# Performance work log

Hardware: AMD Instinct MI355X
Metric: run time of the kernel (lower is better)

The kernel has to match this reference:

```python
import jax, jax.numpy as jnp
import numpy as np

N = 1600        # brain parcellation nodes
MAXD = 500      # delay-buffer length
B = 4           # batches
DT = 0.05
T_STEPS = 500   # steps per batch

# theta layout (ModelParams means):
# 0 std_in, 1 W_E, 2 tau_E, 3 gamma_E, 4 W_I, 5 tau_I, 6 I_0, 7 g,
# 8 g_EE, 9 g_IE, 10 g_EI, 11 aE, 12 bE, 13 dE, 14 aI, 15 bI, 16 dI
THETA = np.array([0.02, 1.0, 100.0, 0.641/1000.0, 0.7, 10.0, 0.32, 20.0,
                  0.1, 0.1, 0.1, 310.0, 125.0, 0.16, 615.0, 177.0, 0.087],
                 dtype=np.float32)


def h_tf(a, b, d, current):
    u = a * current - b
    num = 1e-5 + jnp.abs(u)
    den = 1e-5 * d + jnp.abs(1.0 - jnp.exp(-d * u))
    return num / (den + 1e-8)


def setup_inputs() -> dict:
    key = jax.random.key(0)
    k0, k1, k2, k3, k4 = jax.random.split(key, 5)
    SC = jax.random.uniform(k0, (N, N), dtype=jnp.float32) / N  # normalized connectivity
    L = jnp.diag(SC.sum(axis=1)) - SC                           # graph Laplacian D - SC
    x0 = 0.1 * jax.random.uniform(k1, (N, 2), dtype=jnp.float32)
    hE = 0.1 * jax.random.uniform(k2, (N, MAXD), dtype=jnp.float32)
    delays = jax.random.randint(k3, (N, N), 0, MAXD)
    noise_raw = jax.random.normal(k4, (B, N, 2), dtype=jnp.float32)
    theta = jnp.asarray(THETA)
    return {"x0": x0, "hE": hE, "L": L, "theta": theta,
            "noise_raw": noise_raw, "delays": delays, "batches": B}


def reference(x0, hE, L, theta, noise_raw, delays, batches):
    (std_in, W_E, tau_E, gamma_E, W_I, tau_I, I_0, g,
     g_EE, g_IE, g_EI, aE, bE, dE_c, aI, bI, dI_c) = [theta[i] for i in range(17)]

    def run_batch(x, hEb, noise):
        def step(carry, _):
            x, hEc = carry
            E = x[:, 0:1]
            I = x[:, 1:2]
            # delay gather: out[i,j] = hE[i, delays[i,j]], then mean over j
            delayed_E = jnp.take_along_axis(hEc, delays, axis=1).mean(axis=1, keepdims=True)
            I_E = W_E * I_0 + g_EE * E + g * (L @ delayed_E) - g_IE * I
            I_I = W_I * I_0 + g_EI * E - I
            R_E = h_tf(aE, bE, dE_c, I_E)
            R_I = h_tf(aI, bI, dI_c, I_I)
            dE = -E / tau_E + (1.0 - E) * gamma_E * R_E
            dI = -I / tau_I + R_I
            x_new = x + DT * jnp.concatenate([dE, dI], axis=1) + noise
            hE_new = jnp.concatenate([x_new[:, 0:1], hEc[:, :-1]], axis=1)
            return (x_new, hE_new), x_new

        (x_f, hE_f), ys = jax.lax.scan(step, (x, hEb), None, length=T_STEPS - 1)
        X = jnp.concatenate([x[None], ys], axis=0)  # (T, N, 2)
        return X, x_f, hE_f

    sdt = std_in * jnp.sqrt(jnp.float32(DT))
    x = x0
    Xs = []
    for b in range(batches):  # small fixed count of sequential batches
        X, x, hE = run_batch(x, hE, noise_raw[b] * sdt)
        Xs.append(X)
    X_all = jnp.concatenate(Xs, axis=0)  # (batches*T, N, 2)
    return X_all, x, hE
```

## Files before the change

kernel.cpp:

```cpp
#include <hip/hip_runtime.h>
#include <math.h>

#define NN 1600
#define MAXD 500
#define TS 500
#define NBATCH 4
#define GBLK 100
#define WAVES 4
#define NWAVE (GBLK * WAVES)
#define RPW 4
#define NFLAG 512
#define DT 0.05f

typedef unsigned int u32;


#define ATSF(p,v)  __hip_atomic_store((p), (v), __ATOMIC_RELAXED, __HIP_MEMORY_SCOPE_AGENT)
#define ATSU(p,v)  __hip_atomic_store((p), (v), __ATOMIC_RELAXED, __HIP_MEMORY_SCOPE_AGENT)

__device__ __forceinline__ float h_tf_dev(float a, float b, float d, float c) {
    float u   = a * c - b;
    float num = 1e-5f + fabsf(u);
    float den = 1e-5f * d + fabsf(1.0f - expf(-d * u));
    return num / (den + 1e-8f);
}

__global__ void cnt_kernel(const int* __restrict__ delays, float* __restrict__ cnt) {
    __shared__ int hist[MAXD];
    const int i = blockIdx.x;
    for (int d = threadIdx.x; d < MAXD; d += blockDim.x) hist[d] = 0;
    __syncthreads();
    const int* row = delays + (size_t)i * NN;
    for (int j = threadIdx.x; j < NN; j += blockDim.x) atomicAdd(&hist[row[j]], 1);
    __syncthreads();
    for (int d = threadIdx.x; d < MAXD; d += blockDim.x)
        cnt[(size_t)i * MAXD + d] = (float)hist[d];
}

__global__ void init_kernel(const float* __restrict__ hE, const float* __restrict__ cnt,
                            float* __restrict__ Hc, float* deT, u32* flags) {
    const int i = blockIdx.x;
    const int lane = threadIdx.x;
    float s = 0.f;
    for (int d = lane; d < MAXD; d += 64) {
        float v = hE[(size_t)i * MAXD + d];
        Hc[(size_t)i * MAXD + d] = v;
        s = fmaf(cnt[(size_t)i * MAXD + d], v, s);
    }
    #pragma unroll
    for (int off = 32; off; off >>= 1) s += __shfl_xor(s, off);
    if (lane == 0) ATSF(&deT[i], s / 1600.0f);
    if (i == 0) {
        for (int k = lane; k < NFLAG; k += 64)
            ATSU(&flags[k], (k < NWAVE) ? 0u : 0x7FFFFFFFu);
    }
}

#define ISSUE_DE() do { \
    asm volatile("global_load_dwordx4 %0, %1, off sc0 sc1" : "=v"(q0) : "v"(src + (lane*4         )) : "memory"); \
    asm volatile("global_load_dwordx4 %0, %1, off sc0 sc1" : "=v"(q1) : "v"(src + (lane*4 + 1*256)) : "memory"); \
    asm volatile("global_load_dwordx4 %0, %1, off sc0 sc1" : "=v"(q2) : "v"(src + (lane*4 + 2*256)) : "memory"); \
    asm volatile("global_load_dwordx4 %0, %1, off sc0 sc1" : "=v"(q3) : "v"(src + (lane*4 + 3*256)) : "memory"); \
    asm volatile("global_load_dwordx4 %0, %1, off sc0 sc1" : "=v"(q4) : "v"(src + (lane*4 + 4*256)) : "memory"); \
    asm volatile("global_load_dwordx4 %0, %1, off sc0 sc1" : "=v"(q5) : "v"(src + (lane*4 + 5*256)) : "memory"); \
    asm volatile("global_load_dword %0, %1, off sc0 sc1"   : "=v"(qx) : "v"(src + (1536 + lane   )) : "memory"); \
} while (0)

__global__ __launch_bounds__(256, 1) void dmf_main(
        const float* __restrict__ x0, const float* __restrict__ L,
        const float* __restrict__ theta, const float* __restrict__ noise,
        float* __restrict__ out, const float* __restrict__ cnt,
        float* __restrict__ Hc, float* deT, u32* flags) {
    const int lane = threadIdx.x & 63;
    const int wv   = __builtin_amdgcn_readfirstlane(threadIdx.x >> 6);
    const int widx = blockIdx.x * WAVES + wv;
    const int base = widx * RPW;

    const float std_in = theta[0],  W_E = theta[1],  tau_E = theta[2], gamma_E = theta[3];
    const float W_I = theta[4],     tau_I = theta[5], I_0 = theta[6],  g = theta[7];
    const float g_EE = theta[8],    g_IE = theta[9], g_EI = theta[10];
    const float aE = theta[11], bE = theta[12], dEc = theta[13];
    const float aI = theta[14], bI = theta[15], dIc = theta[16];
    const float sdt = std_in * sqrtf(DT);

    float E = 0.f, I = 0.f, cnt0 = 0.f;
    float* Hmy = Hc;
    if (lane < RPW) {
        const int i = base + lane;
        E = x0[i * 2 + 0];
        I = x0[i * 2 + 1];
        cnt0 = cnt[(size_t)i * MAXD];
        Hmy = Hc + (size_t)i * MAXD;
    }

    float creg[8][RPW];
    #pragma unroll
    for (int k = 0; k < 8; ++k) {
        const int d = lane + k * 64;
        #pragma unroll
        for (int r = 0; r < RPW; ++r)
            creg[k][r] = (d >= 1 && d < MAXD) ? cnt[(size_t)(base + r) * MAXD + d] : 0.f;
    }

    float4 Lreg[RPW][6];
    float  Ltail[RPW];
    #pragma unroll
    for (int r = 0; r < RPW; ++r) {
        #pragma unroll
        for (int k = 0; k < 6; ++k)
            Lreg[r][k] = *(const float4*)&L[(size_t)(base + r) * NN + lane * 4 + k * 256];
        Ltail[r] = L[(size_t)(base + r) * NN + 1536 + lane];
    }

    const u32* fp1 = flags + lane * 4;
    const u32* fp2 = flags + 256 + lane * 4;

    int h = 0;
    u32 e = 0;

    for (int b = 0; b < NBATCH; ++b) {
        float nE = 0.f, nI = 0.f;
        if (lane < RPW) {
            const int i = base + lane;
            nE = noise[((size_t)b * NN + i) * 2 + 0] * sdt;
            nI = noise[((size_t)b * NN + i) * 2 + 1] * sdt;
            ((float2*)out)[(size_t)b * TS * NN + i] = make_float2(E, I);
        }

        for (int t = 1; t < TS; ++t) {
            h = (h == 0) ? (MAXD - 1) : (h - 1);

            float s[RPW];
            #pragma unroll
            for (int r = 0; r < RPW; ++r) s[r] = 0.f;
            #pragma unroll
            for (int k = 0; k < 8; ++k) {
                const int d = lane + k * 64;
                if (d < MAXD) {
                    int hd = h + d; if (hd >= MAXD) hd -= MAXD;
                    #pragma unroll
                    for (int r = 0; r < RPW; ++r)
                        s[r] = fmaf(creg[k][r], Hc[(size_t)(base + r) * MAXD + hd], s[r]);
                }
            }
            #pragma unroll
            for (int off = 32; off; off >>= 1) {
                #pragma unroll
                for (int r = 0; r < RPW; ++r) s[r] += __shfl_xor(s[r], off);
            }
            float sv = s[0];
            #pragma unroll
            for (int r = 1; r < RPW; ++r) sv = (lane == r) ? s[r] : sv;

            {
                const u32 tgt = e;
                for (;;) {
                    uint4 f1, f2;
                    asm volatile("global_load_dwordx4 %0, %1, off sc0 sc1"
                                 : "=v"(f1) : "v"(fp1) : "memory");
                    asm volatile("global_load_dwordx4 %0, %1, off sc0 sc1"
                                 : "=v"(f2) : "v"(fp2) : "memory");
                    asm volatile("s_waitcnt vmcnt(0)" ::: "memory");
                    __builtin_amdgcn_sched_barrier(0);
                    const bool ok = (f1.x >= tgt) & (f1.y >= tgt) & (f1.z >= tgt) & (f1.w >= tgt)
                                  & (f2.x >= tgt) & (f2.y >= tgt) & (f2.z >= tgt) & (f2.w >= tgt);
                    if (__all(ok)) break;
                    __builtin_amdgcn_s_sleep(1);
                }
            }

            const float* src = deT + (size_t)(e & 1) * NN;
            float4 q0, q1, q2, q3, q4, q5;
            float  qx;
            ISSUE_DE();
            asm volatile("s_waitcnt vmcnt(0)" ::: "memory");
            __builtin_amdgcn_sched_barrier(0);

            float p[RPW];
            #pragma unroll
            for (int r = 0; r < RPW; ++r) {
                float acc = 0.f;
                acc = fmaf(Lreg[r][0].x, q0.x, acc); acc = fmaf(Lreg[r][0].y, q0.y, acc);
                acc = fmaf(Lreg[r][0].z, q0.z, acc); acc = fmaf(Lreg[r][0].w, q0.w, acc);
                acc = fmaf(Lreg[r][1].x, q1.x, acc); acc = fmaf(Lreg[r][1].y, q1.y, acc);
                acc = fmaf(Lreg[r][1].z, q1.z, acc); acc = fmaf(Lreg[r][1].w, q1.w, acc);
                acc = fmaf(Lreg[r][2].x, q2.x, acc); acc = fmaf(Lreg[r][2].y, q2.y, acc);
                acc = fmaf(Lreg[r][2].z, q2.z, acc); acc = fmaf(Lreg[r][2].w, q2.w, acc);
                acc = fmaf(Lreg[r][3].x, q3.x, acc); acc = fmaf(Lreg[r][3].y, q3.y, acc);
                acc = fmaf(Lreg[r][3].z, q3.z, acc); acc = fmaf(Lreg[r][3].w, q3.w, acc);
                acc = fmaf(Lreg[r][4].x, q4.x, acc); acc = fmaf(Lreg[r][4].y, q4.y, acc);
                acc = fmaf(Lreg[r][4].z, q4.z, acc); acc = fmaf(Lreg[r][4].w, q4.w, acc);
                acc = fmaf(Lreg[r][5].x, q5.x, acc); acc = fmaf(Lreg[r][5].y, q5.y, acc);
                acc = fmaf(Lreg[r][5].z, q5.z, acc); acc = fmaf(Lreg[r][5].w, q5.w, acc);
                acc = fmaf(Ltail[r], qx, acc);
                p[r] = acc;
            }
            #pragma unroll
            for (int off = 32; off; off >>= 1) {
                #pragma unroll
                for (int r = 0; r < RPW; ++r) p[r] += __shfl_xor(p[r], off);
            }
            float pv = p[0];
            #pragma unroll
            for (int r = 1; r < RPW; ++r) pv = (lane == r) ? p[r] : pv;

            float2 xi;
            if (lane < RPW) {
                const float IE = W_E * I_0 + g_EE * E + g * pv - g_IE * I;
                const float II = W_I * I_0 + g_EI * E - I;
                const float RE = h_tf_dev(aE, bE, dEc, IE);
                const float RI = h_tf_dev(aI, bI, dIc, II);
                const float dEd = -E / tau_E + (1.0f - E) * gamma_E * RE;
                const float dId = -I / tau_I + RI;
                E = E + DT * dEd + nE;
                I = I + DT * dId + nI;
                ATSF(&deT[(size_t)((e + 1) & 1) * NN + base + lane],
                     (sv + cnt0 * E) * (1.0f / 1600.0f));
                xi = make_float2(E, I);
            }
            asm volatile("s_waitcnt vmcnt(0)" ::: "memory");
            __builtin_amdgcn_sched_barrier(0);
            if (lane == 0) ATSU(&flags[widx], e + 1);
            if (lane < RPW) {
                Hmy[h] = E;
                ((float2*)out)[(size_t)(b * TS + t) * NN + base + lane] = xi;
            }
            ++e;
        }
    }

    const size_t xo2 = (size_t)NBATCH * TS * NN;
    if (lane < RPW)
        ((float2*)out)[xo2 + base + lane] = make_float2(E, I);
    const size_t ho = 2 * xo2 + 2 * NN;
    #pragma unroll
    for (int k = 0; k < 8; ++k) {
        const int d = lane + k * 64;
        if (d < MAXD) {
            int hd = h + d; if (hd >= MAXD) hd -= MAXD;
            #pragma unroll
            for (int r = 0; r < RPW; ++r)
                out[ho + (size_t)(base + r) * MAXD + d] =
                    Hc[(size_t)(base + r) * MAXD + hd];
        }
    }
}

extern "C" void kernel_launch(void* const* d_in, const int* in_sizes, int n_in,
                              void* d_out, int out_size, void* d_ws, size_t ws_size,
                              hipStream_t stream) {
    const float* x0     = (const float*)d_in[0];
    const float* hE     = (const float*)d_in[1];
    const float* L      = (const float*)d_in[2];
    const float* theta  = (const float*)d_in[3];
    const float* noise  = (const float*)d_in[4];
    const int*   delays = (const int*)d_in[5];
    float* out = (float*)d_out;

    float* ws  = (float*)d_ws;
    float* cnt = ws;
    float* Hc  = ws + 800000;
    float* deT = ws + 1600000;
    u32*   flags = (u32*)(ws + 1603200);

    cnt_kernel<<<NN, 256, 0, stream>>>(delays, cnt);
    init_kernel<<<NN, 64, 0, stream>>>(hE, cnt, Hc, deT, flags);
    dmf_main<<<GBLK, 256, 0, stream>>>(x0, L, theta, noise, out, cnt, Hc, deT, flags);
}
```

Before: 5.584 ms.

## Tag delayed-E values with parity bits to overlap data loads with flag polling

Each published deT value now carries a parity tag in its mantissa LSB that encodes the step generation. This lets every wave issue its deT loads at the top of the step, ahead of the local delay sum and the flag wait. The flag loads are also issued early, at the end of the previous step. After the flag barrier the wave checks the tags and re-issues the deT loads only if any value is stale, so the load latency overlaps with other work instead of adding a serial round-trip. The cost is one mantissa bit of precision in the delayed-E means and a possible extra retry loop.

```diff
diff --git a/kernel.cpp b/kernel.cpp
--- a/kernel.cpp
+++ b/kernel.cpp
@@ -49,7 +49,11 @@
     }
     #pragma unroll
     for (int off = 32; off; off >>= 1) s += __shfl_xor(s, off);
-    if (lane == 0) ATSF(&deT[i], s / 1600.0f);
+    if (lane == 0) {
+        u32 u = __float_as_uint(s / 1600.0f) & ~1u;
+        ATSF(&deT[i], __uint_as_float(u));
+        ATSF(&deT[NN + i], __uint_as_float(1u));
+    }
     if (i == 0) {
         for (int k = lane; k < NFLAG; k += 64)
             ATSU(&flags[k], (k < NWAVE) ? 0u : 0x7FFFFFFFu);
@@ -66,6 +70,16 @@
     asm volatile("global_load_dword %0, %1, off sc0 sc1"   : "=v"(qx) : "v"(src + (1536 + lane   )) : "memory"); \
 } while (0)
 
+#define ISSUE_FLAGS() do { \
+    asm volatile("global_load_dwordx4 %0, %1, off sc0 sc1" : "=v"(f1) : "v"(fp1) : "memory"); \
+    asm volatile("global_load_dwordx4 %0, %1, off sc0 sc1" : "=v"(f2) : "v"(fp2) : "memory"); \
+} while (0)
+
+#define TAGOK4(Q) (unsigned)( ((__float_as_uint((Q).x) & 1u) == tg) \
+                            & ((__float_as_uint((Q).y) & 1u) == tg) \
+                            & ((__float_as_uint((Q).z) & 1u) == tg) \
+                            & ((__float_as_uint((Q).w) & 1u) == tg) )
+
 __global__ __launch_bounds__(256, 1) void dmf_main(
         const float* __restrict__ x0, const float* __restrict__ L,
         const float* __restrict__ theta, const float* __restrict__ noise,
@@ -118,6 +132,9 @@
     int h = 0;
     u32 e = 0;
 
+    uint4 f1, f2;
+    ISSUE_FLAGS();
+
     for (int b = 0; b < NBATCH; ++b) {
         float nE = 0.f, nI = 0.f;
         if (lane < RPW) {
@@ -130,6 +147,12 @@
         for (int t = 1; t < TS; ++t) {
             h = (h == 0) ? (MAXD - 1) : (h - 1);
 
+            const float* src = deT + (size_t)(e & 1) * NN;
+            const u32 tg = (e >> 1) & 1;
+            float4 q0, q1, q2, q3, q4, q5;
+            float  qx;
+            ISSUE_DE();
+
             float s[RPW];
             #pragma unroll
             for (int r = 0; r < RPW; ++r) s[r] = 0.f;
@@ -155,26 +178,26 @@
             {
                 const u32 tgt = e;
                 for (;;) {
-                    uint4 f1, f2;
-                    asm volatile("global_load_dwordx4 %0, %1, off sc0 sc1"
-                                 : "=v"(f1) : "v"(fp1) : "memory");
-                    asm volatile("global_load_dwordx4 %0, %1, off sc0 sc1"
-                                 : "=v"(f2) : "v"(fp2) : "memory");
                     asm volatile("s_waitcnt vmcnt(0)" ::: "memory");
                     __builtin_amdgcn_sched_barrier(0);
                     const bool ok = (f1.x >= tgt) & (f1.y >= tgt) & (f1.z >= tgt) & (f1.w >= tgt)
                                   & (f2.x >= tgt) & (f2.y >= tgt) & (f2.z >= tgt) & (f2.w >= tgt);
                     if (__all(ok)) break;
                     __builtin_amdgcn_s_sleep(1);
+                    ISSUE_FLAGS();
                 }
             }
 
-            const float* src = deT + (size_t)(e & 1) * NN;
-            float4 q0, q1, q2, q3, q4, q5;
-            float  qx;
-            ISSUE_DE();
-            asm volatile("s_waitcnt vmcnt(0)" ::: "memory");
-            __builtin_amdgcn_sched_barrier(0);
+            for (;;) {
+                unsigned ok = ((__float_as_uint(qx) & 1u) == tg);
+                ok &= TAGOK4(q0); ok &= TAGOK4(q1); ok &= TAGOK4(q2);
+                ok &= TAGOK4(q3); ok &= TAGOK4(q4); ok &= TAGOK4(q5);
+                if (__all(ok)) break;
+                __builtin_amdgcn_s_sleep(1);
+                ISSUE_DE();
+                asm volatile("s_waitcnt vmcnt(0)" ::: "memory");
+                __builtin_amdgcn_sched_barrier(0);
+            }
 
             float p[RPW];
             #pragma unroll
@@ -204,6 +227,7 @@
             #pragma unroll
             for (int r = 1; r < RPW; ++r) pv = (lane == r) ? p[r] : pv;
 
+            const u32 ntg = ((e + 1) >> 1) & 1;
             float2 xi;
             if (lane < RPW) {
                 const float IE = W_E * I_0 + g_EE * E + g * pv - g_IE * I;
@@ -214,8 +238,9 @@
                 const float dId = -I / tau_I + RI;
                 E = E + DT * dEd + nE;
                 I = I + DT * dId + nI;
-                ATSF(&deT[(size_t)((e + 1) & 1) * NN + base + lane],
-                     (sv + cnt0 * E) * (1.0f / 1600.0f));
+                const float val = (sv + cnt0 * E) * (1.0f / 1600.0f);
+                const u32 u = (__float_as_uint(val) & ~1u) | ntg;
+                ATSF(&deT[(size_t)((e + 1) & 1) * NN + base + lane], __uint_as_float(u));
                 xi = make_float2(E, I);
             }
             asm volatile("s_waitcnt vmcnt(0)" ::: "memory");
@@ -225,6 +250,7 @@
                 Hmy[h] = E;
                 ((float2*)out)[(size_t)(b * TS + t) * NN + base + lane] = xi;
             }
+            ISSUE_FLAGS();
             ++e;
         }
     }
```

Measured after the change: 12.31 ms. +120.5%, slower.
